# Optimization experiments

Measured on AMD Instinct MI355X. Metric: run time of the kernel, lower is better.

The kernel has to match this reference:

```python
import jax, jax.numpy as jnp
import numpy as np

D_PARAM = 20   # module's d
S1 = 1         # module's s1
D_WIN = D_PARAM + S1   # 21: sliding-window size -> 441 displacement channels
PAD = D_PARAM // 2     # 10


def setup_inputs() -> dict:
    key = jax.random.key(0)
    k1, k2 = jax.random.split(key)
    B, C, W, H = 4, 128, 128, 128
    x1 = jax.random.normal(k1, (B, C, W, H), dtype=jnp.float32)
    x2 = jax.random.normal(k2, (B, C, W, H), dtype=jnp.float32)
    return {"x1": x1, "x2": x2}


def _correlation(x1, x2):
    # out[b, di*D+dj, i, j] = sum_c x1_padded[b, c, i+di, j+dj] * x2[b, c, i, j]
    # This reproduces: pad x1 by PAD, unfold 21x21 windows stride 1, and for each
    # pixel take the dot product over channels with x2[b,:,i,j] (the 1x1 conv2d
    # in the original triple loop). Flatten order of torch is (di, dj) row-major.
    b, c, w, h = x1.shape
    x1p = jnp.pad(x1, ((0, 0), (0, 0), (PAD, PAD), (PAD, PAD)))  # [b,c,w+20,h+20]
    rows_out = []
    for di in range(D_WIN):  # small fixed displacement loop (21 iters)
        rows = jax.lax.slice_in_dim(x1p, di, di + w, axis=2)  # [b,c,w,h+20]
        # stack 21 horizontal shifts -> [b,c,w,h,D_WIN]
        win = jnp.stack(
            [jax.lax.slice_in_dim(rows, dj, dj + h, axis=3) for dj in range(D_WIN)],
            axis=-1,
        )
        # contract over channels: [b, D_WIN(dj), w, h]
        rows_out.append(jnp.einsum('bcwhd,bcwh->bdwh', win, x2))
    out = jnp.stack(rows_out, axis=1)  # [b, D_WIN(di), D_WIN(dj), w, h]
    return out.reshape(b, D_WIN * D_WIN, w, h)


def reference(x1, x2):
    return _correlation(x1, x2)
```

## Files before the change

kernel.cpp:

```cpp
#include <hip/hip_runtime.h>


#define NB 4
#define NC 128
#define NW 128
#define NH 128
#define DW 21
#define PAD 10
#define NROW_T 148
#define NCOL_T 160
#define NCH 441
#define PS 37
#define SCOLS 52
#define SUS (SCOLS * NC)
#define ROW_US (NCOL_T * NC)

typedef __attribute__((ext_vector_type(8))) short short8;
typedef __attribute__((ext_vector_type(4))) float float4v;

__device__ inline ushort f2bf(float f) {
    union { float f; uint u; } v; v.f = f;
    const uint u = v.u;
    return (ushort)((u + 0x7fffu + ((u >> 16) & 1u)) >> 16);
}

__device__ inline void async_copy16(const void* g, void* l) {
    __builtin_amdgcn_global_load_lds(
        (const __attribute__((address_space(1))) void*)g,
        (__attribute__((address_space(3))) void*)l, 16, 0, 0);
}

__device__ inline void stage_row(const ushort* src, ushort* dst, int t) {
    const char* s = (const char*)src;
    char* d = (char*)dst;
    #pragma unroll
    for (int it = 0; it < 3; ++it) {
        const int off = it * 4096 + t * 16;
        async_copy16(s + off, d + off);
    }
    if (t < 64) {
        const int off = 12288 + t * 16;
        async_copy16(s + off, d + off);
    }
}

__global__ __launch_bounds__(256) void transpose_x1(const float* __restrict__ x1,
                                                    ushort* __restrict__ x1T) {
    __shared__ uint tile[128][65];
    const int t = threadIdx.x;
    const int b = blockIdx.x / NROW_T;
    const int r = blockIdx.x % NROW_T;
    const int w = r - PAD;
    const bool inr = (w >= 0 && w < NW);
    if (inr) {
        #pragma unroll
        for (int it = 0; it < 8; ++it) {
            const int u = it * 256 + t;
            const int g4 = u & 31;
            const int cp = u >> 5;
            const float4 va = *(const float4*)&x1[(((size_t)b * NC + 2 * cp    ) * NW + w) * NH + g4 * 4];
            const float4 vb = *(const float4*)&x1[(((size_t)b * NC + 2 * cp + 1) * NW + w) * NH + g4 * 4];
            tile[g4 * 4 + 0][cp] = (uint)f2bf(va.x) | ((uint)f2bf(vb.x) << 16);
            tile[g4 * 4 + 1][cp] = (uint)f2bf(va.y) | ((uint)f2bf(vb.y) << 16);
            tile[g4 * 4 + 2][cp] = (uint)f2bf(va.z) | ((uint)f2bf(vb.z) << 16);
            tile[g4 * 4 + 3][cp] = (uint)f2bf(va.w) | ((uint)f2bf(vb.w) << 16);
        }
    }
    __syncthreads();
    #pragma unroll
    for (int it = 0; it < 10; ++it) {
        const int u = it * 256 + t;
        const int cg = u & 15;
        const int col = u >> 4;
        uint4 v = make_uint4(0, 0, 0, 0);
        const int h = col - PAD;
        if (inr && h >= 0 && h < NH) {
            v.x = tile[h][cg * 4 + 0];
            v.y = tile[h][cg * 4 + 1];
            v.z = tile[h][cg * 4 + 2];
            v.w = tile[h][cg * 4 + 3];
        }
        const int chunk = cg ^ (col & 15);
        *(uint4*)&x1T[(((size_t)b * NROW_T + r) * NCOL_T + col) * NC + chunk * 8] = v;
    }
}

__global__ __launch_bounds__(256) void corr_mfma(const ushort* __restrict__ x1T,
                                                 const float* __restrict__ x2,
                                                 float* __restrict__ out) {
    __shared__ ushort win[5][SUS];
    __shared__ float patch[4][16 * PS];

    const int t = threadIdx.x;
    const int wave = t >> 6;
    const int lane = t & 63;
    const int n16 = lane & 15;
    const int q = lane >> 4;

    const int n = blockIdx.x;
    const int b = (n & 7) >> 1;
    const int ihalf = n & 1;
    const int slot = n >> 3;
    const int iq = ihalf * 16 + (slot >> 2);
    const int jq = slot & 3;
    const int i0 = iq * 4;
    const int col0 = jq * 32;
    const int i = i0 + wave;

    const ushort* xbase = x1T + (size_t)(b * NROW_T) * ROW_US + (size_t)col0 * NC;

    #pragma unroll
    for (int r = 0; r < 4; ++r)
        stage_row(xbase + (size_t)(i0 + r) * ROW_US, win[r], t);

    short8 Bf[2][4];
    #pragma unroll
    for (int nt = 0; nt < 2; ++nt) {
        const int jc = col0 + nt * 16 + n16;
        #pragma unroll
        for (int k4 = 0; k4 < 4; ++k4) {
            short8 s;
            #pragma unroll
            for (int e = 0; e < 8; ++e) {
                const int c = k4 * 32 + q * 8 + e;
                s[e] = (short)f2bf(x2[(((size_t)b * NC + c) * NW + i) * NH + jc]);
            }
            Bf[nt][k4] = s;
        }
    }

    __syncthreads();

    float* P = &patch[wave][0];

    for (int di = 0; di < DW; ++di) {
        const ushort* A = win[(di + wave) % 5];

        short8 Af[4][4];
        #pragma unroll
        for (int k4 = 0; k4 < 4; ++k4) {
            const int kc = q + 4 * k4;
            #pragma unroll
            for (int tl = 0; tl < 4; ++tl) {
                const int base = (tl < 3) ? tl * 16 : 36;
                const int c = base + n16;
                Af[tl][k4] = *(const short8*)&A[c * NC + ((kc ^ (c & 15)) & 15) * 8];
            }
        }

        if (di < DW - 1)
            stage_row(xbase + (size_t)(i0 + di + 4) * ROW_US, win[(di + 4) % 5], t);

        __builtin_amdgcn_sched_barrier(0);

        float4v a00 = {0.f,0.f,0.f,0.f}, a01 = {0.f,0.f,0.f,0.f}, a02 = {0.f,0.f,0.f,0.f};
        float4v a10 = {0.f,0.f,0.f,0.f}, a11 = {0.f,0.f,0.f,0.f}, a12 = {0.f,0.f,0.f,0.f};
        #pragma unroll
        for (int k4 = 0; k4 < 4; ++k4) {
            a00 = __builtin_amdgcn_mfma_f32_16x16x32_bf16(Af[0][k4], Bf[0][k4], a00, 0, 0, 0);
            a01 = __builtin_amdgcn_mfma_f32_16x16x32_bf16(Af[1][k4], Bf[0][k4], a01, 0, 0, 0);
            a02 = __builtin_amdgcn_mfma_f32_16x16x32_bf16(Af[2][k4], Bf[0][k4], a02, 0, 0, 0);
            a10 = __builtin_amdgcn_mfma_f32_16x16x32_bf16(Af[1][k4], Bf[1][k4], a10, 0, 0, 0);
            a11 = __builtin_amdgcn_mfma_f32_16x16x32_bf16(Af[2][k4], Bf[1][k4], a11, 0, 0, 0);
            a12 = __builtin_amdgcn_mfma_f32_16x16x32_bf16(Af[3][k4], Bf[1][k4], a12, 0, 0, 0);
        }

        #pragma unroll
        for (int nt = 0; nt < 2; ++nt) {
            const float4v va = nt ? a10 : a00;
            const float4v vb = nt ? a11 : a01;
            const float4v vc = nt ? a12 : a02;
            #pragma unroll
            for (int reg = 0; reg < 4; ++reg) {
                P[n16 * PS + q * 4 + reg]      = va[reg];
                P[n16 * PS + 16 + q * 4 + reg] = vb[reg];
            }
            if (q == (nt ? 3 : 0)) {
                #pragma unroll
                for (int reg = 0; reg < 4; ++reg)
                    P[n16 * PS + 32 + reg] = vc[reg];
            }
            #pragma unroll
            for (int it2 = 0; it2 < 2; ++it2) {
                const int u = it2 * 64 + lane;
                if (u < 84) {
                    const int dj = u >> 2;
                    const int jj = (u & 3) * 4;
                    float4v v;
                    #pragma unroll
                    for (int p = 0; p < 4; ++p)
                        v[p] = P[(jj + p) * (PS + 1) + dj];
                    *(float4v*)&out[(((size_t)(b * NCH + di * DW + dj)) * NW + i) * NH
                                    + col0 + nt * 16 + jj] = v;
                }
            }
        }

        asm volatile("s_waitcnt vmcnt(4)" ::: "memory");
        __builtin_amdgcn_s_barrier();
        __builtin_amdgcn_sched_barrier(0);
    }
}

extern "C" void kernel_launch(void* const* d_in, const int* in_sizes, int n_in,
                              void* d_out, int out_size, void* d_ws, size_t ws_size,
                              hipStream_t stream) {
    const float* x1 = (const float*)d_in[0];
    const float* x2 = (const float*)d_in[1];
    float* out = (float*)d_out;
    ushort* x1T = (ushort*)d_ws;
    transpose_x1<<<dim3(NB * NROW_T), dim3(256), 0, stream>>>(x1, x1T);
    corr_mfma<<<dim3(NB * 32 * 4), dim3(256), 0, stream>>>(x1T, x2, out);
}
```

Baseline: 187.6 us.

## Rotate displacement order per wave to share staged rows and shrink LDS ring

Each wave now walks the 21 displacement rows in a rotated order, so at step s all waves read the same staged row from a 3-buffer LDS ring instead of a 5-buffer ring. Waves whose rotated schedule needs rows beyond the staged range read them straight from global memory. The point is to cut LDS use, which may raise occupancy, and to simplify prefetch to two rows ahead. The cost is uncoalesced global A-fragment loads for the wrapped-around rows and more complex vmcnt accounting, which is a correctness risk.

```diff
diff --git a/kernel.cpp b/kernel.cpp
--- a/kernel.cpp
+++ b/kernel.cpp
@@ -14,6 +14,7 @@
 #define SCOLS 52
 #define SUS (SCOLS * NC)
 #define ROW_US (NCOL_T * NC)
+#define NBUF 3
 
 typedef __attribute__((ext_vector_type(8))) short short8;
 typedef __attribute__((ext_vector_type(4))) float float4v;
@@ -88,7 +89,7 @@
 __global__ __launch_bounds__(256) void corr_mfma(const ushort* __restrict__ x1T,
                                                  const float* __restrict__ x2,
                                                  float* __restrict__ out) {
-    __shared__ ushort win[5][SUS];
+    __shared__ ushort win[NBUF][SUS];
     __shared__ float patch[4][16 * PS];
 
     const int t = threadIdx.x;
@@ -109,9 +110,8 @@
 
     const ushort* xbase = x1T + (size_t)(b * NROW_T) * ROW_US + (size_t)col0 * NC;
 
-    #pragma unroll
-    for (int r = 0; r < 4; ++r)
-        stage_row(xbase + (size_t)(i0 + r) * ROW_US, win[r], t);
+    stage_row(xbase + (size_t)(i0 + 0) * ROW_US, win[0], t);
+    stage_row(xbase + (size_t)(i0 + 1) * ROW_US, win[1], t);
 
     short8 Bf[2][4];
     #pragma unroll
@@ -133,23 +133,38 @@
 
     float* P = &patch[wave][0];
 
-    for (int di = 0; di < DW; ++di) {
-        const ushort* A = win[(di + wave) % 5];
+    for (int s = 0; s < 21; ++s) {
+        const int di = (s - wave + 21) % 21;
 
         short8 Af[4][4];
-        #pragma unroll
-        for (int k4 = 0; k4 < 4; ++k4) {
-            const int kc = q + 4 * k4;
-            #pragma unroll
-            for (int tl = 0; tl < 4; ++tl) {
-                const int base = (tl < 3) ? tl * 16 : 36;
-                const int c = base + n16;
-                Af[tl][k4] = *(const short8*)&A[c * NC + ((kc ^ (c & 15)) & 15) * 8];
-            }
-        }
-
-        if (di < DW - 1)
-            stage_row(xbase + (size_t)(i0 + di + 4) * ROW_US, win[(di + 4) % 5], t);
+        if (s >= wave) {
+            const ushort* A = win[s % NBUF];
+            #pragma unroll
+            for (int k4 = 0; k4 < 4; ++k4) {
+                const int kc = q + 4 * k4;
+                #pragma unroll
+                for (int tl = 0; tl < 4; ++tl) {
+                    const int base = (tl < 3) ? tl * 16 : 36;
+                    const int c = base + n16;
+                    Af[tl][k4] = *(const short8*)&A[c * NC + ((kc ^ (c & 15)) & 15) * 8];
+                }
+            }
+        } else {
+            const ushort* A = xbase + (size_t)(i0 + s + 21) * ROW_US;
+            #pragma unroll
+            for (int k4 = 0; k4 < 4; ++k4) {
+                const int kc = q + 4 * k4;
+                #pragma unroll
+                for (int tl = 0; tl < 4; ++tl) {
+                    const int base = (tl < 3) ? tl * 16 : 36;
+                    const int c = base + n16;
+                    Af[tl][k4] = *(const short8*)&A[c * NC + ((kc ^ (c & 15)) & 15) * 8];
+                }
+            }
+        }
+
+        if (s + 2 <= 20)
+            stage_row(xbase + (size_t)(i0 + s + 2) * ROW_US, win[(s + 2) % NBUF], t);
 
         __builtin_amdgcn_sched_barrier(0);
 
@@ -196,9 +211,12 @@
             }
         }
 
-        asm volatile("s_waitcnt vmcnt(4)" ::: "memory");
-        __builtin_amdgcn_s_barrier();
-        __builtin_amdgcn_sched_barrier(0);
+        if (s < 20) {
+            if (s < 19) { asm volatile("s_waitcnt vmcnt(7)" ::: "memory"); }
+            else        { asm volatile("s_waitcnt vmcnt(4)" ::: "memory"); }
+            __builtin_amdgcn_s_barrier();
+            __builtin_amdgcn_sched_barrier(0);
+        }
     }
 }
 
```

Measured after the change: 191.6 us. 1.02x slower.
